# Performance work log

Measured on AMD Instinct MI355X. Metric: run time of the kernel, lower is better.

## Reference

```python
import jax, jax.numpy as jnp
import numpy as np

T = 10          # time_steps
IN_DIM = 784    # 28*28
HID = 256
NCLS = 47
THRESH = 1.0
TAU_MEM = 2.0   # LIF membrane time constant
TAU_OUT = 2.0   # readout EMA time constant


@jax.custom_vjp
def spike_fn(u):
    # Heaviside spike on (v - threshold), surrogate gradient in bwd.
    return (u >= 0.0).astype(u.dtype)

def _spike_fwd(u):
    return spike_fn(u), u

def _spike_bwd(u, g):
    # sigmoid surrogate derivative, slope 4
    s = jax.nn.sigmoid(4.0 * u)
    return (g * 4.0 * s * (1.0 - s),)

spike_fn.defvjp(_spike_fwd, _spike_bwd)


def setup_inputs() -> dict:
    key = jax.random.key(0)
    k1, k2, k3 = jax.random.split(key, 3)
    x = jax.random.uniform(k1, (4096, 1, 28, 28), dtype=jnp.float32)
    W1 = jax.random.normal(k2, (IN_DIM, HID), dtype=jnp.float32) / np.float32(np.sqrt(IN_DIM))
    b1 = jnp.zeros((HID,), jnp.float32)
    Wr = jax.random.normal(k3, (HID, NCLS), dtype=jnp.float32) / np.float32(np.sqrt(HID))
    br = jnp.zeros((NCLS,), jnp.float32)
    return {"x": x, "W1": W1, "b1": b1, "Wr": Wr, "br": br}


def reference(x, W1, b1, Wr, br):
    B = x.shape[0]
    xf = x.reshape(B, -1)  # [B, 784] pixel intensities in [0,1]
    # rate_encode_flat: Bernoulli(p=pixel) spikes per timestep -> [T, B, 784]
    ek = jax.random.key(42)
    seq = (jax.random.uniform(ek, (T, B, IN_DIM), dtype=xf.dtype) < xf[None]).astype(xf.dtype)

    def step(carry, s_t):
        v_hid, v_out = carry
        I_hid = s_t @ W1 + b1                      # [B, HID]
        v_hid = v_hid + (I_hid - v_hid) / TAU_MEM  # leaky integration
        spk = spike_fn(v_hid - THRESH)             # spike emission
        v_hid = v_hid * (1.0 - spk)                # hard reset to 0
        I = spk @ Wr + br                          # [B, NCLS]
        v_out = v_out + (I - v_out) / TAU_OUT      # output EMA
        return (v_hid, v_out), None

    init = (jnp.zeros((B, HID), xf.dtype), jnp.zeros((B, NCLS), xf.dtype))
    (_, v_out), _ = jax.lax.scan(step, init, seq)
    return v_out
```

## Files before the change

kernel.cpp:

```cpp
#include <hip/hip_runtime.h>
#include <stdint.h>


#define T_STEPS 10
#define BATCH   4096
#define IN_DIM  784
#define HID     256
#define NCLS    47
#define KWORDS  25
#define KPAD    800

#define WS_W1HI_OFF 46039040u
#define WS_W1MD_OFF (46039040u + 409600u)
#define WS_W1LO_OFF (46039040u + 819200u)

typedef __attribute__((ext_vector_type(8))) short    bf16x8;
typedef __attribute__((ext_vector_type(4))) float    f32x4;

__device__ __forceinline__ uint32_t rotl32(uint32_t x, uint32_t r) {
    return __builtin_amdgcn_alignbit(x, x, 32u - r);
}

__device__ __forceinline__ uint32_t tf_hash(uint32_t lo) {
    const uint32_t ks1 = 42u;
    const uint32_t ks2 = 0x1BD11BDAu ^ 42u;
    uint32_t x0 = 0u;
    uint32_t x1 = lo + ks1;
#define TF_RND(r) { x0 += x1; x1 = rotl32(x1, r); x1 ^= x0; }
    TF_RND(13) TF_RND(15) TF_RND(26) TF_RND(6)
    x0 += ks1; x1 += ks2 + 1u;
    TF_RND(17) TF_RND(29) TF_RND(16) TF_RND(24)
    x0 += ks2; x1 += 2u;
    TF_RND(13) TF_RND(15) TF_RND(26) TF_RND(6)
    x1 += ks1 + 3u;
    TF_RND(17) TF_RND(29) TF_RND(16) TF_RND(24)
    x0 += ks1; x1 += ks2 + 4u;
    TF_RND(13) TF_RND(15) TF_RND(26) TF_RND(6)
    x0 += ks2; x1 += 5u;
#undef TF_RND
    return x0 ^ x1;
}

__global__ __launch_bounds__(256) void splitk_k(
        const float* __restrict__ W1, ushort* __restrict__ hiT,
        ushort* __restrict__ midT, ushort* __restrict__ loT) {
    int n = blockIdx.x;
    for (int k = threadIdx.x; k < KPAD; k += 256) {
        float w = (k < IN_DIM) ? W1[k * HID + n] : 0.0f;
        uint32_t u = __float_as_uint(w);
        uint32_t hb = (u + 0x7FFFu + ((u >> 16) & 1u)) >> 16;
        float hf = __uint_as_float(hb << 16);
        float r1 = w - hf;
        uint32_t u1 = __float_as_uint(r1);
        uint32_t mb = (u1 + 0x7FFFu + ((u1 >> 16) & 1u)) >> 16;
        float mf2 = __uint_as_float(mb << 16);
        float r2 = r1 - mf2;
        uint32_t u2 = __float_as_uint(r2);
        uint32_t lb = (u2 + 0x7FFFu + ((u2 >> 16) & 1u)) >> 16;
        int kw = k >> 5, qk = (k >> 3) & 3, j = k & 7;
        size_t o = ((size_t)(kw * 256 + n) * 4 + qk) * 8 + j;
        hiT [o] = (ushort)hb;
        midT[o] = (ushort)mb;
        loT [o] = (ushort)lb;
    }
}

#define A_BUFSZ 5120
#define G_LDW   260

__global__ __launch_bounds__(512, 4) void fused_gemm_k(
        const ushort* __restrict__ hiT, const ushort* __restrict__ midT,
        const ushort* __restrict__ loT, const float* __restrict__ b1,
        const float* __restrict__ x, const float* __restrict__ Wr,
        const float* __restrict__ br, float* __restrict__ out) {
    __shared__ __align__(16) char lds[10240];

    const int tid = threadIdx.x;
    const int l   = tid & 63;
    const int wv  = tid >> 6;
    const int b0  = blockIdx.x << 3;

    f32x4 acc[5][2] = {};

    const int q   = l >> 4;
    const int c0  = l & 15;
    const int sig = q ^ (l & 3) ^ ((l >> 2) & 3);
    const int a_rd = (c0 << 6) + (sig << 4);

    const int beoff = ((wv << 5) + c0) * 32 + (q << 3);
    const ushort* bp_hi = hiT  + beoff;
    const ushort* bp_md = midT + beoff;
    const ushort* bp_lo = loT  + beoff;

    const int eL   = tid & 31;
    const int row0 = tid >> 5;
    const int j0   = row0 & 7;
    const int qd0  = ((eL >> 1) >> 2) ^ (row0 & 3) ^ ((row0 >> 2) & 3);
    const int adst0 = (row0 << 6) + (qd0 << 4) + (((eL >> 1) & 3) << 2)
                    + ((eL & 1) << 1);
    const int xbase = (b0 + j0) * IN_DIM + eL;
    const uint32_t tib0 = (uint32_t)((row0 >> 3) * BATCH + b0 + j0)
                        * (uint32_t)IN_DIM + (uint32_t)eL;

#define HASH_SLAB(koff, abase, xv) \
    _Pragma("unroll") \
    for (int s = 0; s < 5; ++s) { \
        uint32_t h = tf_hash(tib0 + (uint32_t)(s * 6422528) + (uint32_t)(koff)); \
        ushort w_ = ((float)(h >> 9) < (xv) * 8388608.0f) ? (ushort)0x3F80 : (ushort)0; \
        *(ushort*)(lds + (abase) + adst0 + (s << 10)) = w_; \
    }

#define PRELOAD_A(bufidx) \
    const char* A = lds + (bufidx) * A_BUFSZ; \
    bf16x8 af[5]; \
    _Pragma("unroll") \
    for (int mt = 0; mt < 5; ++mt) \
        af[mt] = *(const bf16x8*)(A + a_rd + (mt << 10));

#define LOAD_B \
    bf16x8 bfr[3][2]; \
    _Pragma("unroll") \
    for (int nt = 0; nt < 2; ++nt) { \
        bfr[0][nt] = *(const bf16x8*)(bp_hi + nt * 512); \
        bfr[1][nt] = *(const bf16x8*)(bp_md + nt * 512); \
        bfr[2][nt] = *(const bf16x8*)(bp_lo + nt * 512); \
    } \
    bp_hi += 8192; bp_md += 8192; bp_lo += 8192;

#define MFMA_ALL \
    _Pragma("unroll") \
    for (int nt = 0; nt < 2; ++nt) { \
        _Pragma("unroll") \
        for (int mt = 0; mt < 5; ++mt) { \
            acc[mt][nt] = __builtin_amdgcn_mfma_f32_16x16x32_bf16(af[mt], bfr[0][nt], acc[mt][nt], 0, 0, 0); \
            acc[mt][nt] = __builtin_amdgcn_mfma_f32_16x16x32_bf16(af[mt], bfr[1][nt], acc[mt][nt], 0, 0, 0); \
            acc[mt][nt] = __builtin_amdgcn_mfma_f32_16x16x32_bf16(af[mt], bfr[2][nt], acc[mt][nt], 0, 0, 0); \
        } \
    }

    {
        float xv0 = x[xbase];
        HASH_SLAB(0, 0, xv0)
    }
    __syncthreads();

    int cur = 0;
#pragma unroll 1
    for (int kw = 0; kw < KWORDS; ++kw) {
        LOAD_B
        PRELOAD_A(cur)
        if (kw < KWORDS - 1) {
            const int koff = (kw + 1) << 5;
            float xv = 0.0f;
            if (!(kw == KWORDS - 2 && eL >= 16))
                xv = x[xbase + koff];
            HASH_SLAB(koff, (cur ^ 1) * A_BUFSZ, xv)
        }
        MFMA_ALL

        __syncthreads();
        cur ^= 1;
    }
#undef HASH_SLAB
#undef PRELOAD_A
#undef LOAD_B
#undef MFMA_ALL

    float b1v[2];
#pragma unroll
    for (int nt = 0; nt < 2; ++nt)
        b1v[nt] = b1[(wv << 5) + (nt << 4) + c0];

    float av[5][2][4];
#pragma unroll
    for (int mt = 0; mt < 5; ++mt)
#pragma unroll
        for (int nt = 0; nt < 2; ++nt)
#pragma unroll
            for (int rr = 0; rr < 4; ++rr)
                av[mt][nt][rr] = acc[mt][nt][rr] + b1v[nt];

    const int qh = q >> 1;
    float g[2][4];
#pragma unroll
    for (int nt = 0; nt < 2; ++nt) {
#pragma unroll
        for (int rr = 0; rr < 4; ++rr) {
            float v = 0.f, ga = 0.f, wt = 0.0009765625f;
#pragma unroll
            for (int m = 0; m < 5; ++m) {
                float pv = __shfl_xor(av[m][nt][rr], 32);
                float Ie = qh ? pv : av[m][nt][rr];
                float Io = qh ? av[m][nt][rr] : pv;
                v = v + (Ie - v) * 0.5f;
                if (v >= 1.0f) { ga += wt; v = 0.f; }
                wt += wt;
                v = v + (Io - v) * 0.5f;
                if (v >= 1.0f) { ga += wt; v = 0.f; }
                wt += wt;
            }
            g[nt][rr] = ga;
        }
    }

    float* gbuf = (float*)lds;
    if (l < 32) {
#pragma unroll
        for (int nt = 0; nt < 2; ++nt)
#pragma unroll
            for (int rr = 0; rr < 4; ++rr) {
                int jj  = ((q & 1) << 2) + rr;
                int col = (wv << 5) + (nt << 4) + c0;
                gbuf[jj * G_LDW + col] = g[nt][rr];
            }
    }
    __syncthreads();

    {
        const int c = l;
        if (c < NCLS) {
            const float* gb = &gbuf[wv * G_LDW];
            float a = 0.f;
            for (int h4 = 0; h4 < 64; ++h4) {
                float w0 = Wr[((h4 << 2) + 0) * NCLS + c];
                float w1 = Wr[((h4 << 2) + 1) * NCLS + c];
                float w2 = Wr[((h4 << 2) + 2) * NCLS + c];
                float w3 = Wr[((h4 << 2) + 3) * NCLS + c];
                float4 gg = *(const float4*)&gb[h4 << 2];
                a = fmaf(gg.x, w0, a);
                a = fmaf(gg.y, w1, a);
                a = fmaf(gg.z, w2, a);
                a = fmaf(gg.w, w3, a);
            }
            out[(b0 + wv) * NCLS + c] = a + br[c] * 0.9990234375f;
        }
    }
}

extern "C" void kernel_launch(void* const* d_in, const int* in_sizes, int n_in,
                              void* d_out, int out_size, void* d_ws, size_t ws_size,
                              hipStream_t stream) {
    const float* x  = (const float*)d_in[0];
    const float* W1 = (const float*)d_in[1];
    const float* b1 = (const float*)d_in[2];
    const float* Wr = (const float*)d_in[3];
    const float* br = (const float*)d_in[4];
    float* out = (float*)d_out;

    ushort* w1hi  = (ushort*)((char*)d_ws + WS_W1HI_OFF);
    ushort* w1md  = (ushort*)((char*)d_ws + WS_W1MD_OFF);
    ushort* w1lo  = (ushort*)((char*)d_ws + WS_W1LO_OFF);

    splitk_k<<<HID, 256, 0, stream>>>(W1, w1hi, w1md, w1lo);
    fused_gemm_k<<<BATCH / 8, 512, 0, stream>>>(w1hi, w1md, w1lo, b1, x,
                                                Wr, br, out);
}
```

Baseline: 178.6 us.

## Precompute all spike slabs into LDS before a sync-free MFMA loop

Replaces the double-buffered pipeline, which hashed the next K-slab while running MFMAs on the current one and synchronised every iteration, with two phases. First all 25 Bernoulli spike slabs are generated into a 128 KB LDS buffer, then a single barrier, then an MFMA loop with no barriers. This removes 24 per-iteration barriers and the interleaving bookkeeping. In exchange it needs so much LDS that only one 512-thread block fits per CU (launch bounds lowered to 1), so the hash and MFMA phases no longer overlap within or across blocks. A barrier is added before the gbuf reuse of LDS.

```diff
diff --git a/kernel.cpp b/kernel.cpp
--- a/kernel.cpp
+++ b/kernel.cpp
@@ -68,12 +68,12 @@
 #define A_BUFSZ 5120
 #define G_LDW   260
 
-__global__ __launch_bounds__(512, 4) void fused_gemm_k(
+__global__ __launch_bounds__(512, 1) void fused_gemm_k(
         const ushort* __restrict__ hiT, const ushort* __restrict__ midT,
         const ushort* __restrict__ loT, const float* __restrict__ b1,
         const float* __restrict__ x, const float* __restrict__ Wr,
         const float* __restrict__ br, float* __restrict__ out) {
-    __shared__ __align__(16) char lds[10240];
+    __shared__ __align__(16) char lds[KWORDS * A_BUFSZ];
 
     const int tid = threadIdx.x;
     const int l   = tid & 63;
@@ -102,69 +102,54 @@
     const uint32_t tib0 = (uint32_t)((row0 >> 3) * BATCH + b0 + j0)
                         * (uint32_t)IN_DIM + (uint32_t)eL;
 
-#define HASH_SLAB(koff, abase, xv) \
-    _Pragma("unroll") \
-    for (int s = 0; s < 5; ++s) { \
-        uint32_t h = tf_hash(tib0 + (uint32_t)(s * 6422528) + (uint32_t)(koff)); \
-        ushort w_ = ((float)(h >> 9) < (xv) * 8388608.0f) ? (ushort)0x3F80 : (ushort)0; \
-        *(ushort*)(lds + (abase) + adst0 + (s << 10)) = w_; \
-    }
-
-#define PRELOAD_A(bufidx) \
-    const char* A = lds + (bufidx) * A_BUFSZ; \
-    bf16x8 af[5]; \
-    _Pragma("unroll") \
-    for (int mt = 0; mt < 5; ++mt) \
-        af[mt] = *(const bf16x8*)(A + a_rd + (mt << 10));
-
-#define LOAD_B \
-    bf16x8 bfr[3][2]; \
-    _Pragma("unroll") \
-    for (int nt = 0; nt < 2; ++nt) { \
-        bfr[0][nt] = *(const bf16x8*)(bp_hi + nt * 512); \
-        bfr[1][nt] = *(const bf16x8*)(bp_md + nt * 512); \
-        bfr[2][nt] = *(const bf16x8*)(bp_lo + nt * 512); \
-    } \
-    bp_hi += 8192; bp_md += 8192; bp_lo += 8192;
-
-#define MFMA_ALL \
-    _Pragma("unroll") \
-    for (int nt = 0; nt < 2; ++nt) { \
-        _Pragma("unroll") \
-        for (int mt = 0; mt < 5; ++mt) { \
-            acc[mt][nt] = __builtin_amdgcn_mfma_f32_16x16x32_bf16(af[mt], bfr[0][nt], acc[mt][nt], 0, 0, 0); \
-            acc[mt][nt] = __builtin_amdgcn_mfma_f32_16x16x32_bf16(af[mt], bfr[1][nt], acc[mt][nt], 0, 0, 0); \
-            acc[mt][nt] = __builtin_amdgcn_mfma_f32_16x16x32_bf16(af[mt], bfr[2][nt], acc[mt][nt], 0, 0, 0); \
-        } \
-    }
-
     {
-        float xv0 = x[xbase];
-        HASH_SLAB(0, 0, xv0)
+        const float* xp = x + xbase;
+        uint32_t ib = tib0;
+#pragma unroll 1
+        for (int kw = 0; kw < KWORDS; ++kw) {
+            float xv = 0.0f;
+            if (!(kw == KWORDS - 1 && eL >= 16))
+                xv = xp[0];
+            float xs = xv * 8388608.0f;
+            char* ab = lds + kw * A_BUFSZ + adst0;
+#pragma unroll
+            for (int s = 0; s < 5; ++s) {
+                uint32_t h = tf_hash(ib + (uint32_t)(s * 6422528));
+                *(ushort*)(ab + (s << 10)) =
+                    ((float)(h >> 9) < xs) ? (ushort)0x3F80 : (ushort)0;
+            }
+            xp += 32; ib += 32u;
+        }
     }
     __syncthreads();
 
-    int cur = 0;
 #pragma unroll 1
     for (int kw = 0; kw < KWORDS; ++kw) {
-        LOAD_B
-        PRELOAD_A(cur)
-        if (kw < KWORDS - 1) {
-            const int koff = (kw + 1) << 5;
-            float xv = 0.0f;
-            if (!(kw == KWORDS - 2 && eL >= 16))
-                xv = x[xbase + koff];
-            HASH_SLAB(koff, (cur ^ 1) * A_BUFSZ, xv)
-        }
-        MFMA_ALL
-
-        __syncthreads();
-        cur ^= 1;
-    }
-#undef HASH_SLAB
-#undef PRELOAD_A
-#undef LOAD_B
-#undef MFMA_ALL
+        bf16x8 bfr[3][2];
+#pragma unroll
+        for (int nt = 0; nt < 2; ++nt) {
+            bfr[0][nt] = *(const bf16x8*)(bp_hi + nt * 512);
+            bfr[1][nt] = *(const bf16x8*)(bp_md + nt * 512);
+            bfr[2][nt] = *(const bf16x8*)(bp_lo + nt * 512);
+        }
+        bp_hi += 8192; bp_md += 8192; bp_lo += 8192;
+
+        const char* A = lds + kw * A_BUFSZ;
+        bf16x8 af[5];
+#pragma unroll
+        for (int mt = 0; mt < 5; ++mt)
+            af[mt] = *(const bf16x8*)(A + a_rd + (mt << 10));
+
+#pragma unroll
+        for (int nt = 0; nt < 2; ++nt) {
+#pragma unroll
+            for (int mt = 0; mt < 5; ++mt) {
+                acc[mt][nt] = __builtin_amdgcn_mfma_f32_16x16x32_bf16(af[mt], bfr[0][nt], acc[mt][nt], 0, 0, 0);
+                acc[mt][nt] = __builtin_amdgcn_mfma_f32_16x16x32_bf16(af[mt], bfr[1][nt], acc[mt][nt], 0, 0, 0);
+                acc[mt][nt] = __builtin_amdgcn_mfma_f32_16x16x32_bf16(af[mt], bfr[2][nt], acc[mt][nt], 0, 0, 0);
+            }
+        }
+    }
 
     float b1v[2];
 #pragma unroll
@@ -203,6 +188,7 @@
         }
     }
 
+    __syncthreads();
     float* gbuf = (float*)lds;
     if (l < 32) {
 #pragma unroll
```

Measured after the change: 209.3 us. 1.17x slower.
